# Performance work log

Measured on AMD Instinct MI355X. Metric: run time of the kernel, lower is better.

Reference implementation:

```python
import jax, jax.numpy as jnp
import numpy as np

BS = 4
D = 256
N3 = BS * 80 * 80   # 25600 level-3 nodes
N4 = BS * 40 * 40   # 6400  level-4 nodes
N5 = BS * 20 * 20   # 1600  level-5 nodes
N = N3 + N4 + N5    # 33600 total graph nodes
EC = 260000         # contextual-graph edges (~8-neighborhood lattice)
EH = 120000         # hierarchical-graph edges (cross-scale)


def setup_inputs() -> dict:
    key = jax.random.key(0)
    ks = jax.random.split(key, 16)
    f = lambda k, s: jax.random.normal(k, s, dtype=jnp.float32) * 0.05
    return {
        # backbone features (yolov8-l channel widths)
        'c3': f(ks[0], (BS, 256, 80, 80)),
        'c4': f(ks[1], (BS, 512, 40, 40)),
        'c5': f(ks[2], (BS, 512, 20, 20)),
        # lateral 1x1 convs (stored as [out, in] since kernel is 1x1)
        'w3_1x1': f(ks[3], (256, 256)), 'b3_1x1': jnp.zeros((256,), jnp.float32),
        'w4_1x1': f(ks[4], (256, 512)), 'b4_1x1': jnp.zeros((256,), jnp.float32),
        'w5_1x1': f(ks[5], (256, 512)), 'b5_1x1': jnp.zeros((256,), jnp.float32),
        # output 3x3 convs
        'w3_3x3': f(ks[6], (256, 256, 3, 3)), 'b3_3x3': jnp.zeros((256,), jnp.float32),
        'w4_3x3': f(ks[7], (256, 256, 3, 3)), 'b4_3x3': jnp.zeros((256,), jnp.float32),
        'w5_3x3': f(ks[8], (256, 256, 3, 3)), 'b5_3x3': jnp.zeros((256,), jnp.float32),
        # 6 contextual + 3 hierarchical GNN layers (stacked)
        'Wc': f(ks[9], (6, 256, 256)), 'bc': jnp.zeros((6, 256), jnp.float32),
        'Wh': f(ks[10], (3, 256, 256)), 'bh': jnp.zeros((3, 256), jnp.float32),
        # edge lists (src -> dst message direction)
        'src_c': jax.random.randint(ks[11], (EC,), 0, N, dtype=jnp.int32),
        'dst_c': jax.random.randint(ks[12], (EC,), 0, N, dtype=jnp.int32),
        'src_h': jax.random.randint(ks[13], (EH,), 0, N, dtype=jnp.int32),
        'dst_h': jax.random.randint(ks[14], (EH,), 0, N, dtype=jnp.int32),
    }


def _conv1x1(x, w, b):
    return jnp.einsum('bchw,oc->bohw', x, w) + b[None, :, None, None]


def _conv3x3(x, w, b):
    y = jax.lax.conv_general_dilated(x, w, (1, 1), 'SAME')
    return y + b[None, :, None, None]


def _up2(x):
    return jnp.repeat(jnp.repeat(x, 2, axis=2), 2, axis=3)


def _degree(dst):
    d = jax.ops.segment_sum(jnp.ones(dst.shape, jnp.float32), dst, num_segments=N)
    return jnp.maximum(d, 1.0)[:, None]


def _gnn_layer(h, W, b, src, dst, deg):
    # gather-aggregate-scatter: mean over incoming messages + self, then linear+relu
    agg = jax.ops.segment_sum(h[src], dst, num_segments=N) / deg  # [N, D]
    return jax.nn.relu((h + agg) @ W + b)


def reference(c3, c4, c5,
              w3_1x1, b3_1x1, w4_1x1, b4_1x1, w5_1x1, b5_1x1,
              w3_3x3, b3_3x3, w4_3x3, b4_3x3, w5_3x3, b5_3x3,
              Wc, bc, Wh, bh,
              src_c, dst_c, src_h, dst_h):
    p3 = _conv1x1(c3, w3_1x1, b3_1x1)  # [BS,256,80,80]
    p4 = _conv1x1(c4, w4_1x1, b4_1x1)  # [BS,256,40,40]
    p5 = _conv1x1(c5, w5_1x1, b5_1x1)  # [BS,256,20,20]

    # CNN -> graph node features (NHWC flatten, cat levels)
    h = jnp.concatenate([
        p3.transpose(0, 2, 3, 1).reshape(-1, D),
        p4.transpose(0, 2, 3, 1).reshape(-1, D),
        p5.transpose(0, 2, 3, 1).reshape(-1, D),
    ], axis=0)  # [N, 256]

    deg_c = _degree(dst_c)
    deg_h = _degree(dst_h)
    for i in range(3):                       # context1..3
        h = _gnn_layer(h, Wc[i], bc[i], src_c, dst_c, deg_c)
    for i in range(3):                       # hierarch1..3
        h = _gnn_layer(h, Wh[i], bh[i], src_h, dst_h, deg_h)
    for i in range(3, 6):                    # context4..6
        h = _gnn_layer(h, Wc[i], bc[i], src_c, dst_c, deg_c)

    # graph -> CNN
    p3g = h[:N3].reshape(BS, 80, 80, D).transpose(0, 3, 1, 2)
    p4g = h[N3:N3 + N4].reshape(BS, 40, 40, D).transpose(0, 3, 1, 2)
    p5g = h[N3 + N4:].reshape(BS, 20, 20, D).transpose(0, 3, 1, 2)

    p5 = p5 + p5g
    p4 = p4 + _up2(p5) + p4g
    p3 = p3 + _up2(p4) + p3g

    out3 = _conv3x3(p3, w3_3x3, b3_3x3)
    out4 = _conv3x3(p4, w4_3x3, b4_3x3)
    out5 = _conv3x3(p5, w5_3x3, b5_3x3)
    return out3, out4, out5
```

## Files before the change

### kernel.cpp

```cpp
#include <hip/hip_runtime.h>
#include <stdint.h>

#define N3i 25600
#define N4i 6400
#define N5i 1600
#define NNi 33600
#define ECi 260000
#define EHi 120000

typedef unsigned short u16;
typedef __bf16 bf16x8 __attribute__((ext_vector_type(8)));
typedef float f32x4 __attribute__((ext_vector_type(4)));
typedef unsigned short u16x8 __attribute__((ext_vector_type(8)));

__device__ __forceinline__ float b2f(u16 u) {
    union { float f; uint32_t i; } v; v.i = ((uint32_t)u) << 16; return v.f;
}
__device__ __forceinline__ u16 f2b(float f) {
    union { float f; uint32_t i; } v; v.f = f;
    uint32_t x = v.i;
    uint32_t r = (x + 0x7FFFu + ((x >> 16) & 1u)) >> 16;
    return (u16)r;
}

__device__ __forceinline__ void gll16(const u16* g, u16* l) {
    __builtin_amdgcn_global_load_lds((const __attribute__((address_space(1))) void*)g,
                                     (__attribute__((address_space(3))) void*)l, 16, 0, 0);
}

__device__ __forceinline__ bool xcd_pair_decode(int pid, int& p, int& x) {
    int g = pid & 7;
    int s = pid >> 3;
    x = s & 1;
    p = g * 33 + (s >> 1);
    return p < 263;
}

__global__ void detect_kernel(const void* __restrict__ c3raw, int* __restrict__ flag,
                              uint32_t* __restrict__ zp) {
    const uint32_t* p = (const uint32_t*)c3raw;
    int t = threadIdx.x;
    zp[t] = 0;
    zp[t + 64] = 0;
    int vote = 0;
    for (int i = t; i < 256; i += 64) {
        uint32_t w = p[i];
        uint32_t lo = w & 0xFFFFu;
        uint32_t e = (lo >> 7) & 0xFFu;
        if (lo == 0u || (e >= 100u && e <= 127u)) vote++;
    }
#pragma unroll
    for (int d = 32; d >= 1; d >>= 1) vote += __shfl_down(vote, d, 64);
    if (t == 0) flag[0] = (vote >= 192) ? 1 : 0;
}

__global__ void zero_i32(int* p, int n) {
    int i = blockIdx.x * 256 + threadIdx.x;
    if (i < n) p[i] = 0;
}

__global__ void hist2_kernel(const int* __restrict__ dst_c, const int* __restrict__ dst_h,
                             int* __restrict__ cnt_c, int* __restrict__ cnt_h) {
    int i = blockIdx.x * 256 + threadIdx.x;
    if (i < ECi) {
        int d = dst_c[i];
        if ((unsigned)d < (unsigned)NNi) atomicAdd(&cnt_c[d], 1);
    } else {
        int j = i - ECi;
        if (j < EHi) {
            int d = dst_h[j];
            if ((unsigned)d < (unsigned)NNi) atomicAdd(&cnt_h[d], 1);
        }
    }
}

__global__ __launch_bounds__(256) void scan_part(
    const int* __restrict__ cnt_c, const int* __restrict__ cnt_h,
    int* __restrict__ ps_c, int* __restrict__ ps_h, int* __restrict__ bsum) {
    int b = blockIdx.x;
    bool hier = b >= 66;
    const int* cnt = hier ? cnt_h : cnt_c;
    int* ps = hier ? ps_h : ps_c;
    int base = (hier ? b - 66 : b) * 512;
    int t = threadIdx.x, lane = t & 63, wid = t >> 6;
    int i0 = base + 2 * t;
    int v0 = (i0 < NNi) ? cnt[i0] : 0;
    int v1 = (i0 + 1 < NNi) ? cnt[i0 + 1] : 0;
    int s = v0 + v1;
    int x = s;
#pragma unroll
    for (int d = 1; d < 64; d <<= 1) {
        int y = __shfl_up(x, d, 64);
        if (lane >= d) x += y;
    }
    __shared__ int ws[4];
    if (lane == 63) ws[wid] = x;
    __syncthreads();
    int w0 = ws[0], w1 = ws[1], w2 = ws[2], w3 = ws[3];
    int woff = (wid == 1) ? w0 : (wid == 2) ? (w0 + w1) : (wid == 3) ? (w0 + w1 + w2) : 0;
    int incl = x + woff;
    int excl = incl - s;
    if (i0 < NNi) ps[i0] = excl + v0;
    if (i0 + 1 < NNi) ps[i0 + 1] = excl + v0 + v1;
    if (t == 0) bsum[b] = w0 + w1 + w2 + w3;
}

__global__ __launch_bounds__(256) void scan_sums(int* __restrict__ bsum) {
    __shared__ int s[132];
    int t = threadIdx.x;
    int orig = 0;
    if (t < 132) { orig = bsum[t]; s[t] = orig; }
    __syncthreads();
    for (int d = 1; d < 66; d <<= 1) {
        int v = 0;
        if (t < 132) {
            int seg = (t < 66) ? 0 : 1;
            int loc = t - seg * 66;
            if (loc >= d) v = s[t - d];
        }
        __syncthreads();
        if (t < 132) s[t] += v;
        __syncthreads();
    }
    if (t < 132) bsum[t] = s[t] - orig;
}

__global__ __launch_bounds__(256) void scan_final(
    const int* __restrict__ ps_c, const int* __restrict__ ps_h, const int* __restrict__ bsum,
    const int* __restrict__ cnt_c, const int* __restrict__ cnt_h,
    int* __restrict__ rs_c, int* __restrict__ cur_c, float* __restrict__ inv_c,
    int* __restrict__ rs_h, int* __restrict__ cur_h, float* __restrict__ inv_h) {
    int b = blockIdx.x;
    bool hier = b >= 66;
    int lb = hier ? b - 66 : b;
    const int* ps = hier ? ps_h : ps_c;
    const int* cnt = hier ? cnt_h : cnt_c;
    int* rs = hier ? rs_h : rs_c;
    int* cur = hier ? cur_h : cur_c;
    float* inv = hier ? inv_h : inv_c;
    int off = bsum[b];
    int t = threadIdx.x;
#pragma unroll
    for (int k = 0; k < 2; k++) {
        int i = lb * 512 + t + k * 256;
        if (i < NNi) {
            int incl = ps[i] + off;
            int v = cnt[i];
            rs[i + 1] = incl;
            cur[i] = incl - v;
            inv[i] = 1.0f / (float)(v < 1 ? 1 : v);
        }
    }
    if (b == 0 && t == 0) rs_c[0] = 0;
    if (b == 66 && t == 0) rs_h[0] = 0;
}

__global__ void fill2_kernel(const int* __restrict__ src_c, const int* __restrict__ dst_c,
                             int* __restrict__ cur_c, int* __restrict__ csr_c,
                             const int* __restrict__ src_h, const int* __restrict__ dst_h,
                             int* __restrict__ cur_h, int* __restrict__ csr_h) {
    int i = blockIdx.x * 256 + threadIdx.x;
    if (i < ECi) {
        int d = dst_c[i];
        if ((unsigned)d < (unsigned)NNi) {
            int p = atomicAdd(&cur_c[d], 1);
            if ((unsigned)p < (unsigned)ECi) csr_c[p] = src_c[i];
        }
    } else {
        int j = i - ECi;
        if (j < EHi) {
            int d = dst_h[j];
            if ((unsigned)d < (unsigned)NNi) {
                int p = atomicAdd(&cur_h[d], 1);
                if ((unsigned)p < (unsigned)EHi) csr_h[p] = src_h[j];
            }
        }
    }
}

struct CvtJobs { const void* src[11]; u16* dst[11]; int n[11]; };

__global__ void cvt_all_kernel(CvtJobs j, const int* __restrict__ flag) {
    int job = blockIdx.y;
    int i = blockIdx.x * 256 + threadIdx.x;
    if (i >= j.n[job]) return;
    const void* s = j.src[job];
    j.dst[job][i] = flag[0] ? ((const u16*)s)[i] : f2b(((const float*)s)[i]);
}

__device__ __forceinline__ void tin_body(const void* in, size_t ioff, u16* outp, int R, int C,
                                         int isb, int c0, int r0, u16 (*tile)[33]) {
    const u16* inb = (const u16*)in + ioff;
    const float* inf_ = (const float*)in + ioff;
    int tx = threadIdx.x, ty = threadIdx.y;
#pragma unroll
    for (int i = 0; i < 4; i++) {
        int r = r0 + ty + i * 8, c = c0 + tx;
        if (r < R && c < C) {
            size_t idx = (size_t)r * C + c;
            tile[ty + i * 8][tx] = isb ? inb[idx] : f2b(inf_[idx]);
        }
    }
    __syncthreads();
#pragma unroll
    for (int i = 0; i < 4; i++) {
        int c = c0 + ty + i * 8, r = r0 + tx;
        if (c < C && r < R) outp[(size_t)c * R + r] = tile[tx][ty + i * 8];
    }
}

__global__ void transpose_in3(const void* __restrict__ c3, const void* __restrict__ c4,
                              const void* __restrict__ c5, u16* __restrict__ Xt3,
                              u16* __restrict__ Xt4, u16* __restrict__ Xt5,
                              const int* __restrict__ flag) {
    __shared__ u16 tile[32][33];
    int bx = blockIdx.x;
    const void* in; u16* outb; int R, C, xb;
    if (bx < 200)      { in = c3; outb = Xt3; R = 256; C = 6400; xb = bx; }
    else if (bx < 250) { in = c4; outb = Xt4; R = 512; C = 1600; xb = bx - 200; }
    else               { in = c5; outb = Xt5; R = 512; C = 400;  xb = bx - 250; }
    int r0 = blockIdx.y * 32;
    if (r0 >= R) return;
    size_t boff = (size_t)blockIdx.z * R * C;
    tin_body(in, boff, outb + boff, R, C, flag[0], xb * 32, r0, tile);
}

__global__ void transpose_w(const void* __restrict__ Wc, const void* __restrict__ Wh,
                            u16* __restrict__ WtG, const int* __restrict__ flag) {
    __shared__ u16 tile[32][33];
    int z = blockIdx.z;
    const void* in = (z < 6) ? Wc : Wh;
    int zi = (z < 6) ? z : z - 6;
    tin_body(in, (size_t)zi * 65536, WtG + (size_t)z * 65536, 256, 256, flag[0],
             blockIdx.x * 32, blockIdx.y * 32, tile);
}

__global__ void transpose_out3(const u16* __restrict__ OutT, void* __restrict__ outv,
                               const int* __restrict__ flag) {
    __shared__ u16 tile[32][33];
    int by = blockIdx.y;
    const u16* inb; size_t out_off; int R, yb;
    if (by < 200)      { inb = OutT; out_off = 0; R = 6400; yb = by; }
    else if (by < 250) { inb = OutT + (size_t)N3i * 256; out_off = (size_t)4 * 256 * 6400; R = 1600; yb = by - 200; }
    else               { inb = OutT + (size_t)(N3i + N4i) * 256; out_off = (size_t)4 * 256 * 8000; R = 400; yb = by - 250; }
    int r0 = yb * 32;
    if (r0 >= R) return;
    const int C = 256;
    int isb = flag[0];
    int c0 = blockIdx.x * 32;
    size_t boff = (size_t)blockIdx.z * R * C;
    const u16* inp = inb + boff;
    int tx = threadIdx.x, ty = threadIdx.y;
#pragma unroll
    for (int i = 0; i < 4; i++) {
        int r = r0 + ty + i * 8, c = c0 + tx;
        if (r < R && c < C) tile[ty + i * 8][tx] = inp[(size_t)r * C + c];
    }
    __syncthreads();
#pragma unroll
    for (int i = 0; i < 4; i++) {
        int c = c0 + ty + i * 8, r = r0 + tx;
        if (c < C && r < R) {
            size_t o = out_off + boff + (size_t)c * R + r;
            u16 v = tile[tx][ty + i * 8];
            if (isb) ((u16*)outv)[o] = v;
            else ((float*)outv)[o] = b2f(v);
        }
    }
}

__global__ void convw3_kernel(const void* __restrict__ w0, const void* __restrict__ w1,
                              const void* __restrict__ w2, u16* __restrict__ WtC,
                              const int* __restrict__ flag) {
    int lvl = blockIdx.y;
    const void* w = (lvl == 0) ? w0 : (lvl == 1) ? w1 : w2;
    u16* wt = WtC + (size_t)lvl * 256 * 2304;
    int i = blockIdx.x * 256 + threadIdx.x;
    if (i >= 256 * 2304) return;
    int n = i / 2304;
    int k = i - n * 2304;
    int tap = k >> 8, ci = k & 255;
    int si = n * 2304 + ci * 9 + tap;
    wt[i] = flag[0] ? ((const u16*)w)[si] : f2b(((const float*)w)[si]);
}

__global__ __launch_bounds__(256) void gather_kernel(
    const u16* __restrict__ H, const int* __restrict__ csr, const int* __restrict__ rs,
    const float* __restrict__ invdeg, u16* __restrict__ T, const u16* __restrict__ zp,
    int ecap) {
    int bid = blockIdx.x;
    int nb = (bid & 7) * 525 + (bid >> 3);
    int node = nb * 8 + (threadIdx.x >> 5);
    if (node >= NNi) return;
    int L = threadIdx.x & 31;
    int c = L * 8;
    int e0 = rs[node], e1 = rs[node + 1];
    e0 = e0 < 0 ? 0 : e0;
    e1 = e1 > ecap ? ecap : e1;
    u16x8 self = *(const u16x8*)(H + (size_t)node * 256 + c);
    const u16* zrow = zp + c;
    float a0 = 0.f, a1 = 0.f, a2 = 0.f, a3 = 0.f, a4 = 0.f, a5 = 0.f, a6 = 0.f, a7 = 0.f;
    for (int base = e0; base < e1; base += 32) {
        int ee = base + L;
        int iv = -1;
        if (ee < e1) {
            iv = csr[ee];
            if ((unsigned)iv >= (unsigned)NNi) iv = -1;
        }
        int cnt = e1 - base;
        cnt = cnt > 32 ? 32 : cnt;
        for (int k = 0; k < cnt; k += 8) {
            u16x8 hv[8];
#pragma unroll
            for (int u = 0; u < 8; u++) {
                int j = __shfl(iv, k + u, 32);
                bool val = (k + u < cnt) && (j >= 0);
                const u16* ptr = val ? (H + (size_t)j * 256 + c) : zrow;
                hv[u] = *(const u16x8*)ptr;
            }
#pragma unroll
            for (int u = 0; u < 8; u++) {
                a0 += b2f(hv[u][0]); a1 += b2f(hv[u][1]);
                a2 += b2f(hv[u][2]); a3 += b2f(hv[u][3]);
                a4 += b2f(hv[u][4]); a5 += b2f(hv[u][5]);
                a6 += b2f(hv[u][6]); a7 += b2f(hv[u][7]);
            }
        }
    }
    float inv = invdeg[node];
    u16x8 o;
    o[0] = f2b(b2f(self[0]) + a0 * inv); o[1] = f2b(b2f(self[1]) + a1 * inv);
    o[2] = f2b(b2f(self[2]) + a2 * inv); o[3] = f2b(b2f(self[3]) + a3 * inv);
    o[4] = f2b(b2f(self[4]) + a4 * inv); o[5] = f2b(b2f(self[5]) + a5 * inv);
    o[6] = f2b(b2f(self[6]) + a6 * inv); o[7] = f2b(b2f(self[7]) + a7 * inv);
    *(u16x8*)(T + (size_t)node * 256 + c) = o;
}

template <bool CONV, bool RELU>
__device__ __forceinline__ void gemm_body(
    u16 (* __restrict__ lds)[4096],
    const u16* __restrict__ A, int lda,
    const u16* __restrict__ Bt, int ldb,
    const u16* __restrict__ bias,
    const u16* __restrict__ zp,
    u16* __restrict__ out, u16* __restrict__ out2,
    int M, int K, int H, int W, int m0, int n0) {
    int t = threadIdx.x;
    int w = t >> 6, lane = t & 63;
    int wm = w & 1, wn = w >> 1;
    f32x4 acc[4][4] = {};

    int g0 = w * 128 + lane;
    int g1 = g0 + 64;
    int row0 = g0 >> 2, c0 = g0 & 3;
    int row1 = g1 >> 2, c1 = g1 & 3;
    int ss0 = ((c0 ^ ((row0 >> 1) & 3)) << 3);
    int ss1 = ((c1 ^ ((row1 >> 1) & 3)) << 3);

    int ar0 = m0 + row0, ar1 = m0 + row1;
    bool aok0 = ar0 < M, aok1 = ar1 < M;
    int y0_ = 0, x0_ = 0, y1_ = 0, x1_ = 0;
    if (CONV) {
        int HW = H * W;
        if (aok0) { int b = ar0 / HW; int rem = ar0 - b * HW; y0_ = rem / W; x0_ = rem - y0_ * W; }
        if (aok1) { int b = ar1 / HW; int rem = ar1 - b * HW; y1_ = rem / W; x1_ = rem - y1_ * W; }
    }
    const u16* aP0 = A + (size_t)ar0 * lda + ss0;
    const u16* aP1 = A + (size_t)ar1 * lda + ss1;
    const u16* bP0 = Bt + (size_t)(n0 + row0) * ldb + ss0;
    const u16* bP1 = Bt + (size_t)(n0 + row1) * ldb + ss1;

    int lbase = w * 1024;

    auto stage = [&](int bf, int k0) {
        u16* LA = lds[bf * 2];
        u16* LB = lds[bf * 2 + 1];
        const u16* sa0;
        const u16* sa1;
        if (!CONV) {
            sa0 = aok0 ? aP0 + k0 : zp;
            sa1 = aok1 ? aP1 + k0 : zp;
        } else {
            int tap = k0 >> 8;
            int t3 = tap / 3;
            int dy = t3 - 1, dx = tap - t3 * 3 - 1;
            int off = (dy * W + dx) * lda + (k0 & 255);
            int yy0 = y0_ + dy, xx0 = x0_ + dx;
            int yy1 = y1_ + dy, xx1 = x1_ + dx;
            sa0 = (aok0 && (unsigned)yy0 < (unsigned)H && (unsigned)xx0 < (unsigned)W) ? aP0 + off : zp;
            sa1 = (aok1 && (unsigned)yy1 < (unsigned)H && (unsigned)xx1 < (unsigned)W) ? aP1 + off : zp;
        }
        gll16(sa0, LA + lbase);
        gll16(sa1, LA + lbase + 512);
        gll16(bP0 + k0, LB + lbase);
        gll16(bP1 + k0, LB + lbase + 512);
    };

    int nst = K >> 5;
    int fm = lane & 15;
    int co = (((lane >> 4) ^ ((fm >> 1) & 3)) << 3);

    stage(0, 0);
    __syncthreads();
    for (int s = 0; s < nst; s++) {
        int bf = s & 1;
        if (s + 1 < nst) stage(bf ^ 1, (s + 1) << 5);
        const u16* LA = lds[bf * 2];
        const u16* LB = lds[bf * 2 + 1];
        bf16x8 af[4], bfv[4];
#pragma unroll
        for (int i = 0; i < 4; i++) af[i] = *(const bf16x8*)&LA[(wm * 64 + i * 16 + fm) * 32 + co];
#pragma unroll
        for (int j = 0; j < 4; j++) bfv[j] = *(const bf16x8*)&LB[(wn * 64 + j * 16 + fm) * 32 + co];
#pragma unroll
        for (int i = 0; i < 4; i++)
#pragma unroll
            for (int j = 0; j < 4; j++)
                acc[i][j] = __builtin_amdgcn_mfma_f32_16x16x32_bf16(af[i], bfv[j], acc[i][j], 0, 0, 0);
        __syncthreads();
    }

    int q = lane >> 4, nl = lane & 15;
#pragma unroll
    for (int j = 0; j < 4; j++) {
        int n = n0 + wn * 64 + j * 16 + nl;
        float bv = b2f(bias[n]);
#pragma unroll
        for (int i = 0; i < 4; i++) {
            int mbase = m0 + wm * 64 + i * 16 + q * 4;
#pragma unroll
            for (int rg = 0; rg < 4; rg++) {
                int m = mbase + rg;
                if (m < M) {
                    float v = acc[i][j][rg] + bv;
                    if (RELU) v = fmaxf(v, 0.f);
                    u16 bs = f2b(v);
                    out[(size_t)m * 256 + n] = bs;
                    if (out2) out2[(size_t)m * 256 + n] = bs;
                }
            }
        }
    }
}

template <bool CONV, bool RELU>
__global__ __launch_bounds__(256) void gemm_kernel(
    const u16* __restrict__ A, int lda,
    const u16* __restrict__ Bt, int ldb,
    const u16* __restrict__ bias,
    const u16* __restrict__ zp,
    u16* __restrict__ out, u16* __restrict__ out2,
    int M, int K, int H, int W) {
    __shared__ __align__(16) u16 lds[4][4096];
    int p, x;
    if (!xcd_pair_decode(blockIdx.x, p, x)) return;
    gemm_body<CONV, RELU>(lds, A, lda, Bt, ldb, bias, zp, out, out2, M, K, H, W,
                          p * 128, x * 128);
}

__global__ __launch_bounds__(256) void lat_all_kernel(
    const u16* __restrict__ Xt3, const u16* __restrict__ Xt4, const u16* __restrict__ Xt5,
    const u16* __restrict__ W1, const u16* __restrict__ BB, const u16* __restrict__ zp,
    u16* __restrict__ P, u16* __restrict__ Ha) {
    __shared__ __align__(16) u16 lds[4][4096];
    int p, x;
    if (!xcd_pair_decode(blockIdx.x, p, x)) return;
    const u16* A; const u16* Bt; const u16* bias;
    int K, Ml, m0; size_t off;
    if (p < 200)      { A = Xt3; Bt = W1;          bias = BB;       K = 256; Ml = N3i; off = 0;                          m0 = p * 128; }
    else if (p < 250) { A = Xt4; Bt = W1 + 65536;  bias = BB + 256; K = 512; Ml = N4i; off = (size_t)N3i * 256;          m0 = (p - 200) * 128; }
    else              { A = Xt5; Bt = W1 + 196608; bias = BB + 512; K = 512; Ml = N5i; off = (size_t)(N3i + N4i) * 256;  m0 = (p - 250) * 128; }
    gemm_body<false, false>(lds, A, K, Bt, K, bias, zp, P + off, Ha + off, Ml, K, 0, 0,
                            m0, x * 128);
}

__global__ __launch_bounds__(256) void conv_gemm_all(
    const u16* __restrict__ Pc, const u16* __restrict__ WtC,
    const u16* __restrict__ BB, const u16* __restrict__ zp, u16* __restrict__ OutT) {
    __shared__ __align__(16) u16 lds[4][4096];
    int p, x;
    if (!xcd_pair_decode(blockIdx.x, p, x)) return;
    int lvl, yl, Hd, Ml; size_t base;
    if (p < 200)      { lvl = 0; yl = p;       Hd = 80; Ml = N3i; base = 0; }
    else if (p < 250) { lvl = 1; yl = p - 200; Hd = 40; Ml = N4i; base = (size_t)N3i * 256; }
    else              { lvl = 2; yl = p - 250; Hd = 20; Ml = N5i; base = (size_t)(N3i + N4i) * 256; }
    gemm_body<true, false>(lds, Pc + base, 256, WtC + (size_t)lvl * 256 * 2304, 2304,
                           BB + 3072 + lvl * 256, zp, OutT + base, nullptr,
                           Ml, 2304, Hd, Hd, yl * 128, x * 128);
}

__global__ void pyr_kernel(const u16* __restrict__ P, const u16* __restrict__ Hf,
                           u16* __restrict__ Pc) {
    int i = blockIdx.x * 256 + threadIdx.x;
    if (i >= NNi * 64) return;
    int node = i >> 6, c = (i & 63) * 4;
    size_t bi = (size_t)node * 256 + c;
    ushort4 pv = *(const ushort4*)(P + bi);
    ushort4 hv = *(const ushort4*)(Hf + bi);
    float v0 = b2f(pv.x) + b2f(hv.x);
    float v1 = b2f(pv.y) + b2f(hv.y);
    float v2 = b2f(pv.z) + b2f(hv.z);
    float v3 = b2f(pv.w) + b2f(hv.w);
    if (node < N3i) {
        int b = node / 6400, rem = node - b * 6400;
        int y = rem / 80, x = rem - y * 80;
        size_t s4 = ((size_t)N3i + b * 1600 + (y >> 1) * 40 + (x >> 1)) * 256 + c;
        size_t s5 = ((size_t)(N3i + N4i) + b * 400 + (y >> 2) * 20 + (x >> 2)) * 256 + c;
        ushort4 p4 = *(const ushort4*)(P + s4), h4 = *(const ushort4*)(Hf + s4);
        ushort4 p5 = *(const ushort4*)(P + s5), h5 = *(const ushort4*)(Hf + s5);
        v0 += b2f(p4.x) + b2f(h4.x) + b2f(p5.x) + b2f(h5.x);
        v1 += b2f(p4.y) + b2f(h4.y) + b2f(p5.y) + b2f(h5.y);
        v2 += b2f(p4.z) + b2f(h4.z) + b2f(p5.z) + b2f(h5.z);
        v3 += b2f(p4.w) + b2f(h4.w) + b2f(p5.w) + b2f(h5.w);
    } else if (node < N3i + N4i) {
        int n4 = node - N3i;
        int b = n4 / 1600, rem = n4 - b * 1600;
        int y = rem / 40, x = rem - y * 40;
        size_t s5 = ((size_t)(N3i + N4i) + b * 400 + (y >> 1) * 20 + (x >> 1)) * 256 + c;
        ushort4 p5 = *(const ushort4*)(P + s5), h5 = *(const ushort4*)(Hf + s5);
        v0 += b2f(p5.x) + b2f(h5.x);
        v1 += b2f(p5.y) + b2f(h5.y);
        v2 += b2f(p5.z) + b2f(h5.z);
        v3 += b2f(p5.w) + b2f(h5.w);
    }
    ushort4 o;
    o.x = f2b(v0); o.y = f2b(v1); o.z = f2b(v2); o.w = f2b(v3);
    *(ushort4*)(Pc + bi) = o;
}

extern "C" void kernel_launch(void* const* d_in, const int* in_sizes, int n_in,
                              void* d_out, int out_size, void* d_ws, size_t ws_size,
                              hipStream_t stream) {
    (void)in_sizes; (void)n_in; (void)out_size; (void)ws_size;
    const void* c3 = d_in[0];
    const void* c4 = d_in[1];
    const void* c5 = d_in[2];
    const void* w3_1 = d_in[3];
    const void* b3_1 = d_in[4];
    const void* w4_1 = d_in[5];
    const void* b4_1 = d_in[6];
    const void* w5_1 = d_in[7];
    const void* b5_1 = d_in[8];
    const void* w3_3 = d_in[9];
    const void* b3_3 = d_in[10];
    const void* w4_3 = d_in[11];
    const void* b4_3 = d_in[12];
    const void* w5_3 = d_in[13];
    const void* b5_3 = d_in[14];
    const void* Wc = d_in[15];
    const void* bc = d_in[16];
    const void* Wh = d_in[17];
    const void* bh = d_in[18];
    const int* src_c = (const int*)d_in[19];
    const int* dst_c = (const int*)d_in[20];
    const int* src_h = (const int*)d_in[21];
    const int* dst_h = (const int*)d_in[22];

    char* w = (char*)d_ws;
    auto alloc = [&](size_t bytes) -> void* {
        void* p = (void*)w;
        w += (bytes + 255) & ~(size_t)255;
        return p;
    };
    u16* XT  = (u16*)alloc(((size_t)N3i * 256 + (size_t)N4i * 512 + (size_t)N5i * 512) * 2);
    u16* Xt3 = XT;
    u16* Xt4 = XT + (size_t)N3i * 256;
    u16* Xt5 = Xt4 + (size_t)N4i * 512;
    u16* T   = XT;
    u16* Pc  = XT;
    u16* WtC = XT + (size_t)NNi * 256;
    u16* WtG = (u16*)alloc((size_t)9 * 65536 * 2);
    u16* W1  = (u16*)alloc((size_t)(65536 + 131072 + 131072) * 2);
    u16* BB  = (u16*)alloc((size_t)3840 * 2);
    u16* P   = (u16*)alloc((size_t)NNi * 256 * 2);
    u16* Ha  = (u16*)alloc((size_t)NNi * 256 * 2);
    u16* Hb  = (u16*)d_out;
    int* csr_c = (int*)alloc((size_t)ECi * 4);
    int* csr_h = (int*)alloc((size_t)EHi * 4);
    int* cnt2  = (int*)alloc((size_t)2 * NNi * 4);
    int* cnt_c = cnt2;
    int* cnt_h = cnt2 + NNi;
    int* rs_c  = (int*)alloc((size_t)(NNi + 1) * 4);
    int* rs_h  = (int*)alloc((size_t)(NNi + 1) * 4);
    int* cur_c = (int*)alloc((size_t)NNi * 4);
    int* cur_h = (int*)alloc((size_t)NNi * 4);
    float* inv_c = (float*)alloc((size_t)NNi * 4);
    float* inv_h = (float*)alloc((size_t)NNi * 4);
    int* ps_c  = (int*)alloc((size_t)NNi * 4);
    int* ps_h  = (int*)alloc((size_t)NNi * 4);
    int* bsum  = (int*)alloc((size_t)132 * 4);
    int* flag  = (int*)alloc(256);
    u16* zp    = (u16*)alloc(512);

    detect_kernel<<<1, 64, 0, stream>>>(c3, flag, (uint32_t*)zp);

    zero_i32<<<(2 * NNi + 255) / 256, 256, 0, stream>>>(cnt2, 2 * NNi);
    hist2_kernel<<<(ECi + EHi + 255) / 256, 256, 0, stream>>>(dst_c, dst_h, cnt_c, cnt_h);
    scan_part<<<132, 256, 0, stream>>>(cnt_c, cnt_h, ps_c, ps_h, bsum);
    scan_sums<<<1, 256, 0, stream>>>(bsum);
    scan_final<<<132, 256, 0, stream>>>(ps_c, ps_h, bsum, cnt_c, cnt_h,
                                        rs_c, cur_c, inv_c, rs_h, cur_h, inv_h);
    fill2_kernel<<<(ECi + EHi + 255) / 256, 256, 0, stream>>>(
        src_c, dst_c, cur_c, csr_c, src_h, dst_h, cur_h, csr_h);

    CvtJobs cj;
    cj.src[0] = w3_1; cj.dst[0] = W1;          cj.n[0] = 65536;
    cj.src[1] = w4_1; cj.dst[1] = W1 + 65536;  cj.n[1] = 131072;
    cj.src[2] = w5_1; cj.dst[2] = W1 + 196608; cj.n[2] = 131072;
    cj.src[3] = b3_1; cj.dst[3] = BB;          cj.n[3] = 256;
    cj.src[4] = b4_1; cj.dst[4] = BB + 256;    cj.n[4] = 256;
    cj.src[5] = b5_1; cj.dst[5] = BB + 512;    cj.n[5] = 256;
    cj.src[6] = bc;   cj.dst[6] = BB + 768;    cj.n[6] = 1536;
    cj.src[7] = bh;   cj.dst[7] = BB + 2304;   cj.n[7] = 768;
    cj.src[8] = b3_3; cj.dst[8] = BB + 3072;   cj.n[8] = 256;
    cj.src[9] = b4_3; cj.dst[9] = BB + 3328;   cj.n[9] = 256;
    cj.src[10] = b5_3; cj.dst[10] = BB + 3584; cj.n[10] = 256;
    cvt_all_kernel<<<dim3(512, 11), 256, 0, stream>>>(cj, flag);

    transpose_in3<<<dim3(263, 16, 4), dim3(32, 8), 0, stream>>>(c3, c4, c5, Xt3, Xt4, Xt5, flag);
    transpose_w<<<dim3(8, 8, 9), dim3(32, 8), 0, stream>>>(Wc, Wh, WtG, flag);

    lat_all_kernel<<<528, 256, 0, stream>>>(Xt3, Xt4, Xt5, W1, BB, zp, P, Ha);

    convw3_kernel<<<dim3(2304, 3), 256, 0, stream>>>(w3_3, w4_3, w5_3, WtC, flag);

    u16* Hcur = Ha;
    u16* Hnxt = Hb;
    for (int l = 0; l < 9; l++) {
        bool ctx = (l < 3) || (l >= 6);
        const int* csr = ctx ? csr_c : csr_h;
        const int* rs = ctx ? rs_c : rs_h;
        const float* inv = ctx ? inv_c : inv_h;
        int ecap = ctx ? ECi : EHi;
        int wi = (l < 3) ? l : (l < 6 ? 6 + (l - 3) : l - 3);
        const u16* bias = (l < 3) ? BB + 768 + l * 256
                        : (l < 6 ? BB + 2304 + (l - 3) * 256 : BB + 768 + (l - 3) * 256);
        gather_kernel<<<NNi / 8, 256, 0, stream>>>(Hcur, csr, rs, inv, T, zp, ecap);
        gemm_kernel<false, true><<<528, 256, 0, stream>>>(
            T, 256, WtG + (size_t)wi * 65536, 256, bias, zp, Hnxt, nullptr, NNi, 256, 0, 0);
        u16* tmp = Hcur; Hcur = Hnxt; Hnxt = tmp;
    }
    u16* OutT = Hnxt;

    pyr_kernel<<<(NNi * 64 + 255) / 256, 256, 0, stream>>>(P, Hcur, Pc);

    conv_gemm_all<<<528, 256, 0, stream>>>(Pc, WtC, BB, zp, OutT);

    transpose_out3<<<dim3(8, 263, 4), dim3(32, 8), 0, stream>>>(OutT, d_out, flag);
}
```

Baseline: 621.6 us.

## Merge setup kernels and vectorize transpose stores

Folds the detect and zero kernels into a single prep kernel, and folds the block-sum scan into scan_final so each block redoes the tiny 132-entry scan in shared memory. Two launches are removed from the setup chain. The input and output transposes now read and write four elements per thread with ushort4 and float4 accesses instead of scalar strided stores, which should improve global memory coalescing. The tin_body vector store drops the per-row bounds check and assumes R and the tile start are multiples of four and aligned, and the LDS reads down tile columns may cause bank conflicts.

```diff
diff --git a/kernel.cpp b/kernel.cpp
--- a/kernel.cpp
+++ b/kernel.cpp
@@ -36,27 +36,27 @@
     return p < 263;
 }
 
-__global__ void detect_kernel(const void* __restrict__ c3raw, int* __restrict__ flag,
-                              uint32_t* __restrict__ zp) {
-    const uint32_t* p = (const uint32_t*)c3raw;
-    int t = threadIdx.x;
-    zp[t] = 0;
-    zp[t + 64] = 0;
-    int vote = 0;
-    for (int i = t; i < 256; i += 64) {
-        uint32_t w = p[i];
-        uint32_t lo = w & 0xFFFFu;
-        uint32_t e = (lo >> 7) & 0xFFu;
-        if (lo == 0u || (e >= 100u && e <= 127u)) vote++;
-    }
-#pragma unroll
-    for (int d = 32; d >= 1; d >>= 1) vote += __shfl_down(vote, d, 64);
-    if (t == 0) flag[0] = (vote >= 192) ? 1 : 0;
-}
-
-__global__ void zero_i32(int* p, int n) {
+__global__ void prep_kernel(int* __restrict__ cnt2, int n, const void* __restrict__ c3raw,
+                            int* __restrict__ flag, uint32_t* __restrict__ zp) {
     int i = blockIdx.x * 256 + threadIdx.x;
-    if (i < n) p[i] = 0;
+    if (i < n) cnt2[i] = 0;
+    if (blockIdx.x == 0) {
+        int t = threadIdx.x;
+        if (t < 128) zp[t] = 0;
+        if (t < 64) {
+            const uint32_t* p = (const uint32_t*)c3raw;
+            int vote = 0;
+            for (int k = t; k < 256; k += 64) {
+                uint32_t w = p[k];
+                uint32_t lo = w & 0xFFFFu;
+                uint32_t e = (lo >> 7) & 0xFFu;
+                if (lo == 0u || (e >= 100u && e <= 127u)) vote++;
+            }
+#pragma unroll
+            for (int d = 32; d >= 1; d >>= 1) vote += __shfl_down(vote, d, 64);
+            if (t == 0) flag[0] = (vote >= 192) ? 1 : 0;
+        }
+    }
 }
 
 __global__ void hist2_kernel(const int* __restrict__ dst_c, const int* __restrict__ dst_h,
@@ -105,31 +105,25 @@
     if (t == 0) bsum[b] = w0 + w1 + w2 + w3;
 }
 
-__global__ __launch_bounds__(256) void scan_sums(int* __restrict__ bsum) {
-    __shared__ int s[132];
-    int t = threadIdx.x;
-    int orig = 0;
-    if (t < 132) { orig = bsum[t]; s[t] = orig; }
-    __syncthreads();
-    for (int d = 1; d < 66; d <<= 1) {
-        int v = 0;
-        if (t < 132) {
-            int seg = (t < 66) ? 0 : 1;
-            int loc = t - seg * 66;
-            if (loc >= d) v = s[t - d];
-        }
-        __syncthreads();
-        if (t < 132) s[t] += v;
-        __syncthreads();
-    }
-    if (t < 132) bsum[t] = s[t] - orig;
-}
-
 __global__ __launch_bounds__(256) void scan_final(
     const int* __restrict__ ps_c, const int* __restrict__ ps_h, const int* __restrict__ bsum,
     const int* __restrict__ cnt_c, const int* __restrict__ cnt_h,
     int* __restrict__ rs_c, int* __restrict__ cur_c, float* __restrict__ inv_c,
     int* __restrict__ rs_h, int* __restrict__ cur_h, float* __restrict__ inv_h) {
+    __shared__ int s[132];
+    int t = threadIdx.x;
+    if (t < 132) s[t] = bsum[t];
+    __syncthreads();
+    for (int d = 1; d < 66; d <<= 1) {
+        int v = 0;
+        if (t < 132) {
+            int seg0 = (t < 66) ? 0 : 66;
+            if (t - seg0 >= d) v = s[t - d];
+        }
+        __syncthreads();
+        if (t < 132) s[t] += v;
+        __syncthreads();
+    }
     int b = blockIdx.x;
     bool hier = b >= 66;
     int lb = hier ? b - 66 : b;
@@ -138,8 +132,7 @@
     int* rs = hier ? rs_h : rs_c;
     int* cur = hier ? cur_h : cur_c;
     float* inv = hier ? inv_h : inv_c;
-    int off = bsum[b];
-    int t = threadIdx.x;
+    int off = s[b] - bsum[b];
 #pragma unroll
     for (int k = 0; k < 2; k++) {
         int i = lb * 512 + t + k * 256;
@@ -192,7 +185,8 @@
                                          int isb, int c0, int r0, u16 (*tile)[33]) {
     const u16* inb = (const u16*)in + ioff;
     const float* inf_ = (const float*)in + ioff;
-    int tx = threadIdx.x, ty = threadIdx.y;
+    int t = threadIdx.y * 32 + threadIdx.x;
+    int tx = t & 31, ty = t >> 5;
 #pragma unroll
     for (int i = 0; i < 4; i++) {
         int r = r0 + ty + i * 8, c = c0 + tx;
@@ -202,10 +196,15 @@
         }
     }
     __syncthreads();
-#pragma unroll
-    for (int i = 0; i < 4; i++) {
-        int c = c0 + ty + i * 8, r = r0 + tx;
-        if (c < C && r < R) outp[(size_t)c * R + r] = tile[tx][ty + i * 8];
+    int cidx = t >> 3, r4 = (t & 7) << 2;
+    int c = c0 + cidx;
+    if (c < C) {
+        ushort4 v;
+        v.x = tile[r4][cidx];
+        v.y = tile[r4 + 1][cidx];
+        v.z = tile[r4 + 2][cidx];
+        v.w = tile[r4 + 3][cidx];
+        *(ushort4*)&outp[(size_t)c * R + r0 + r4] = v;
     }
 }
 
@@ -250,21 +249,38 @@
     int c0 = blockIdx.x * 32;
     size_t boff = (size_t)blockIdx.z * R * C;
     const u16* inp = inb + boff;
-    int tx = threadIdx.x, ty = threadIdx.y;
-#pragma unroll
-    for (int i = 0; i < 4; i++) {
-        int r = r0 + ty + i * 8, c = c0 + tx;
-        if (r < R && c < C) tile[ty + i * 8][tx] = inp[(size_t)r * C + c];
+    int t = threadIdx.y * 32 + threadIdx.x;
+    int ridx = t >> 3, c4 = (t & 7) << 2;
+    if (r0 + ridx < R) {
+        ushort4 lv = *(const ushort4*)&inp[(size_t)(r0 + ridx) * C + c0 + c4];
+        tile[ridx][c4] = lv.x; tile[ridx][c4 + 1] = lv.y;
+        tile[ridx][c4 + 2] = lv.z; tile[ridx][c4 + 3] = lv.w;
     }
     __syncthreads();
-#pragma unroll
-    for (int i = 0; i < 4; i++) {
-        int c = c0 + ty + i * 8, r = r0 + tx;
-        if (c < C && r < R) {
-            size_t o = out_off + boff + (size_t)c * R + r;
-            u16 v = tile[tx][ty + i * 8];
-            if (isb) ((u16*)outv)[o] = v;
-            else ((float*)outv)[o] = b2f(v);
+    int cidx = t >> 3, r4 = (t & 7) << 2;
+    int c = c0 + cidx;
+    size_t obase = out_off + boff + (size_t)c * R + r0 + r4;
+    if (r0 + r4 + 3 < R) {
+        if (isb) {
+            ushort4 v;
+            v.x = tile[r4][cidx]; v.y = tile[r4 + 1][cidx];
+            v.z = tile[r4 + 2][cidx]; v.w = tile[r4 + 3][cidx];
+            *(ushort4*)&((u16*)outv)[obase] = v;
+        } else {
+            float4 v;
+            v.x = b2f(tile[r4][cidx]); v.y = b2f(tile[r4 + 1][cidx]);
+            v.z = b2f(tile[r4 + 2][cidx]); v.w = b2f(tile[r4 + 3][cidx]);
+            *(float4*)&((float*)outv)[obase] = v;
+        }
+    } else {
+#pragma unroll
+        for (int k = 0; k < 4; k++) {
+            int r = r0 + r4 + k;
+            if (r < R) {
+                u16 v = tile[r4 + k][cidx];
+                if (isb) ((u16*)outv)[obase + k] = v;
+                else ((float*)outv)[obase + k] = b2f(v);
+            }
         }
     }
 }
@@ -592,12 +608,11 @@
     int* flag  = (int*)alloc(256);
     u16* zp    = (u16*)alloc(512);
 
-    detect_kernel<<<1, 64, 0, stream>>>(c3, flag, (uint32_t*)zp);
-
-    zero_i32<<<(2 * NNi + 255) / 256, 256, 0, stream>>>(cnt2, 2 * NNi);
+    prep_kernel<<<(2 * NNi + 255) / 256, 256, 0, stream>>>(cnt2, 2 * NNi, c3, flag,
+                                                           (uint32_t*)zp);
+
     hist2_kernel<<<(ECi + EHi + 255) / 256, 256, 0, stream>>>(dst_c, dst_h, cnt_c, cnt_h);
     scan_part<<<132, 256, 0, stream>>>(cnt_c, cnt_h, ps_c, ps_h, bsum);
-    scan_sums<<<1, 256, 0, stream>>>(bsum);
     scan_final<<<132, 256, 0, stream>>>(ps_c, ps_h, bsum, cnt_c, cnt_h,
                                         rs_c, cur_c, inv_c, rs_h, cur_h, inv_h);
     fill2_kernel<<<(ECi + EHi + 255) / 256, 256, 0, stream>>>(
```

After: 619.5 us. Within noise of the previous version (-0.3%).
